# Performance work log

Measured on AMD Instinct MI355X. Metric: run time of the kernel, lower is better.

Reference implementation:

```python
import jax, jax.numpy as jnp
import numpy as np

HEADS = 16
HEAD_DIM = 64
HIDDEN = HEADS * HEAD_DIM  # 1024
COMPRESSION = 1.0  # concat([o, p], -1) forces compressed seq len == T, i.e. scale 1
LN_EPS = 1e-5


def _interp_linear_seq(x, scale):
    # F.interpolate(mode='linear', align_corners=False) along the sequence axis.
    # x: [B, T, C] -> [B, int(T*scale), C]
    T = x.shape[1]
    S = int(T * scale)
    src = (jnp.arange(S, dtype=jnp.float32) + 0.5) / scale - 0.5
    src = jnp.clip(src, 0.0, T - 1)
    lo = jnp.floor(src).astype(jnp.int32)
    hi = jnp.minimum(lo + 1, T - 1)
    w = (src - lo.astype(jnp.float32))[None, :, None]
    return x[:, lo] * (1.0 - w) + x[:, hi] * w


def _rotary(x):
    # rotate-half rotary embedding; x: [B, S, h, d]
    S, d = x.shape[1], x.shape[3]
    inv_freq = 1.0 / (10000.0 ** (jnp.arange(0, d, 2, dtype=jnp.float32) / d))
    ang = jnp.arange(S, dtype=jnp.float32)[:, None] * inv_freq  # [S, d/2]
    cos = jnp.cos(ang)[None, :, None, :]
    sin = jnp.sin(ang)[None, :, None, :]
    x1, x2 = jnp.split(x, 2, axis=-1)
    return jnp.concatenate([x1 * cos - x2 * sin, x1 * sin + x2 * cos], axis=-1)


def setup_inputs() -> dict:
    key = jax.random.key(0)
    ks = jax.random.split(key, 4)
    B, T = 4, 2048
    x = jax.random.normal(ks[0], (B, T, HIDDEN), dtype=jnp.float32)
    ln_gamma = jnp.ones((HIDDEN,), dtype=jnp.float32)
    ln_beta = jnp.zeros((HIDDEN,), dtype=jnp.float32)
    w_in = jax.random.normal(ks[1], (HIDDEN, 7 * HIDDEN), dtype=jnp.float32) * (HIDDEN ** -0.5)
    w_out = jax.random.normal(ks[2], (5 * HIDDEN, HIDDEN), dtype=jnp.float32) * ((5 * HIDDEN) ** -0.5)
    b_out = jnp.zeros((HIDDEN,), dtype=jnp.float32)
    return {"x": x, "ln_gamma": ln_gamma, "ln_beta": ln_beta,
            "w_in": w_in, "w_out": w_out, "b_out": b_out}


def reference(x, ln_gamma, ln_beta, w_in, w_out, b_out):
    B, T, _ = x.shape
    # LayerNorm
    mu = jnp.mean(x, axis=-1, keepdims=True)
    var = jnp.mean(jnp.square(x - mu), axis=-1, keepdims=True)
    xn = (x - mu) / jnp.sqrt(var + LN_EPS) * ln_gamma + ln_beta
    # fused QKVP projection (no bias)
    qkvp = xn @ w_in  # [B, T, 7*HIDDEN]
    q, k, v, p = jnp.split(qkvp, [HIDDEN, 2 * HIDDEN, 3 * HIDDEN], axis=-1)
    # linear-interpolation compression of k, v, p along the sequence axis
    k = _interp_linear_seq(k, COMPRESSION)
    v = _interp_linear_seq(v, COMPRESSION)
    p = _interp_linear_seq(p, COMPRESSION)
    S = k.shape[1]
    q = q.reshape(B, T, HEADS, HEAD_DIM)
    k = k.reshape(B, S, HEADS, HEAD_DIM)
    v = v.reshape(B, S, HEADS, HEAD_DIM)
    q = _rotary(q)
    k = _rotary(k)
    # manual softmax attention (no mask in the original)
    a = jnp.einsum('bihd,bjhd->bhij', q, k) * (HEAD_DIM ** -0.5)
    a = jax.nn.softmax(a, axis=-1)
    o = jnp.einsum('bhij,bjhd->bihd', a, v).reshape(B, T, HIDDEN)
    # GELU side branch (torch F.gelu default = exact erf gelu)
    p = jax.nn.gelu(p, approximate=False)
    return jnp.concatenate([o, p], axis=-1) @ w_out + b_out
```

## Files before the change

kernel.cpp:

```cpp
#include <hip/hip_runtime.h>
#include <hip/hip_bf16.h>
#include <math.h>

typedef short bf16x8 __attribute__((ext_vector_type(8)));
typedef float f32x4 __attribute__((ext_vector_type(4)));

#define HEADS 16
#define HDIM 64
#define HID 1024
#define B_ 4
#define T_ 2048
#define BT_ (B_*T_)
#define N1 (7*HID)
#define K2 (5*HID)

#define SM_SCALE_LOG2E 0.18033688011111793f

__device__ __forceinline__ float bf2f(unsigned short u) {
  union { unsigned int i; float f; } c; c.i = ((unsigned int)u) << 16; return c.f;
}
__device__ __forceinline__ unsigned short f2bf(float f) {
  __hip_bfloat16 h = __float2bfloat16(f);
  return __builtin_bit_cast(unsigned short, h);
}

typedef __attribute__((address_space(1))) const unsigned int gu32;
typedef __attribute__((address_space(3))) unsigned int lu32;
__device__ __forceinline__ void async16(const void* g, void* l) {
  __builtin_amdgcn_global_load_lds((gu32*)g, (lu32*)l, 16, 0, 0);
}

__global__ __launch_bounds__(256) void tcast_kernel(const float* __restrict__ in,
                                                    unsigned short* __restrict__ out,
                                                    int R, int C) {
  __shared__ float tile[64][65];
  int tx = threadIdx.x & 63;
  int ty = threadIdx.x >> 6;
  long r0 = (long)blockIdx.y * 64;
  long c0 = (long)blockIdx.x * 64;
#pragma unroll
  for (int i = 0; i < 16; i++) {
    int r = ty + i * 4;
    tile[r][tx] = in[(r0 + r) * C + c0 + tx];
  }
  __syncthreads();
#pragma unroll
  for (int i = 0; i < 16; i++) {
    int rr = ty + i * 4;
    out[(c0 + rr) * R + r0 + tx] = f2bf(tile[tx][rr]);
  }
}

__global__ __launch_bounds__(256) void ln_kernel(const float* __restrict__ x,
                                                 const float* __restrict__ g,
                                                 const float* __restrict__ b,
                                                 unsigned short* __restrict__ xn) {
  int row = blockIdx.x, tid = threadIdx.x;
  float4 v = reinterpret_cast<const float4*>(x + (long)row * HID)[tid];
  float s = v.x + v.y + v.z + v.w;
  float sq = v.x * v.x + v.y * v.y + v.z * v.z + v.w * v.w;
#pragma unroll
  for (int off = 32; off > 0; off >>= 1) { s += __shfl_down(s, off); sq += __shfl_down(sq, off); }
  __shared__ float red[8];
  int wid = tid >> 6, lane = tid & 63;
  if (lane == 0) { red[wid] = s; red[4 + wid] = sq; }
  __syncthreads();
  if (tid == 0) {
    red[0] = red[0] + red[1] + red[2] + red[3];
    red[4] = red[4] + red[5] + red[6] + red[7];
  }
  __syncthreads();
  float mean = red[0] * (1.f / HID);
  float var  = red[4] * (1.f / HID) - mean * mean;
  float rstd = rsqrtf(var + 1e-5f);
  float4 gv = reinterpret_cast<const float4*>(g)[tid];
  float4 bv = reinterpret_cast<const float4*>(b)[tid];
  ushort4 o;
  o.x = f2bf((v.x - mean) * rstd * gv.x + bv.x);
  o.y = f2bf((v.y - mean) * rstd * gv.y + bv.y);
  o.z = f2bf((v.z - mean) * rstd * gv.z + bv.z);
  o.w = f2bf((v.w - mean) * rstd * gv.w + bv.w);
  reinterpret_cast<ushort4*>(xn + (long)row * HID)[tid] = o;
}

__global__ __launch_bounds__(256) void gemm1_fused(const unsigned short* __restrict__ A,
                                                   const unsigned short* __restrict__ BT,
                                                   unsigned short* __restrict__ q_r,
                                                   unsigned short* __restrict__ k_r,
                                                   unsigned short* __restrict__ v_t,
                                                   unsigned short* __restrict__ C5) {
  __shared__ unsigned short As[128 * 32];
  __shared__ unsigned short Bs[128 * 32];
  __shared__ unsigned short Vt[4][64 * 72];
  int tid = threadIdx.x, lane = tid & 63, wid = tid >> 6;
  long row0 = (long)blockIdx.y * 128;
  long col0 = (long)blockIdx.x * 128;
  f32x4 acc[4][4] = {};
  int srow = lane >> 2;
  int scol = (lane & 3) * 8;
  for (int k0 = 0; k0 < HID; k0 += 32) {
#pragma unroll
    for (int i = 0; i < 2; i++) {
      int c = wid * 2 + i;
      async16(A  + (row0 + c * 16 + srow) * (long)HID + k0 + scol, &As[c * 512]);
      async16(BT + (col0 + c * 16 + srow) * (long)HID + k0 + scol, &Bs[c * 512]);
    }
    __syncthreads();
    int wm = (wid & 1) * 64, wn = (wid >> 1) * 64;
    bf16x8 af[4], bfv[4];
#pragma unroll
    for (int m = 0; m < 4; m++)
      af[m] = *reinterpret_cast<const bf16x8*>(&As[(wm + m * 16 + (lane & 15)) * 32 + (lane >> 4) * 8]);
#pragma unroll
    for (int n = 0; n < 4; n++)
      bfv[n] = *reinterpret_cast<const bf16x8*>(&Bs[(wn + n * 16 + (lane & 15)) * 32 + (lane >> 4) * 8]);
#pragma unroll
    for (int m = 0; m < 4; m++)
#pragma unroll
      for (int n = 0; n < 4; n++)
        acc[m][n] = __builtin_amdgcn_mfma_f32_16x16x32_bf16(af[m], bfv[n], acc[m][n], 0, 0, 0);
    __syncthreads();
  }
  int wm = (wid & 1) * 64, wn = (wid >> 1) * 64;
  long row_base = row0 + wm;
  int b = (int)(row_base >> 11);
  int t_base = (int)(row_base & 2047);
  int col_base = (int)col0 + wn;
  int region = col_base >> 10;
  int l15 = lane & 15, lq = lane >> 4;

  if (region <= 1) {
    unsigned short* dst = (region == 0) ? q_r : k_r;
    float osc = (region == 0) ? SM_SCALE_LOG2E : 1.0f;
    int head = (col_base & 1023) >> 6;
    long obase = (long)(b * 16 + head) * T_ * 64;
    float fr[2];
    fr[0] = __expf(-(float)l15 * 0.28782313662425572f);
    fr[1] = __expf(-(float)(16 + l15) * 0.28782313662425572f);
#pragma unroll
    for (int m = 0; m < 4; m++) {
#pragma unroll
      for (int j = 0; j < 4; j++) {
        int t = t_base + m * 16 + lq * 4 + j;
#pragma unroll
        for (int n = 0; n < 2; n++) {
          float sn, cs;
          sincosf((float)t * fr[n], &sn, &cs);
          float xl = acc[m][n][j], xh = acc[m][n + 2][j];
          int d = n * 16 + l15;
          dst[obase + (long)t * 64 + d]      = f2bf((xl * cs - xh * sn) * osc);
          dst[obase + (long)t * 64 + d + 32] = f2bf((xl * sn + xh * cs) * osc);
        }
      }
    }
  } else if (region == 2) {
    int head = (col_base & 1023) >> 6;
    unsigned short* vt = &Vt[wid][0];
#pragma unroll
    for (int m = 0; m < 4; m++)
#pragma unroll
      for (int n = 0; n < 4; n++)
#pragma unroll
        for (int j = 0; j < 4; j++)
          vt[(n * 16 + l15) * 72 + m * 16 + lq * 4 + j] = f2bf(acc[m][n][j]);
    long obase = (long)(b * 16 + head) * 64 * T_;
#pragma unroll
    for (int i = 0; i < 8; i++) {
      int d = i * 8 + (lane >> 3);
      int tl = (lane & 7) * 8;
      bf16x8 v = *reinterpret_cast<const bf16x8*>(&vt[d * 72 + tl]);
      *reinterpret_cast<bf16x8*>(v_t + obase + (long)d * T_ + t_base + tl) = v;
    }
  } else {
    int colp = col_base - 3 * HID;
#pragma unroll
    for (int m = 0; m < 4; m++) {
#pragma unroll
      for (int j = 0; j < 4; j++) {
        long row = row_base + m * 16 + lq * 4 + j;
#pragma unroll
        for (int n = 0; n < 4; n++) {
          float a = acc[m][n][j];
          float ga = 0.5f * a * (1.f + erff(a * 0.70710678118f));
          C5[row * K2 + HID + colp + n * 16 + l15] = f2bf(ga);
        }
      }
    }
  }
}

__global__ __launch_bounds__(256) void gemm_bt(const unsigned short* __restrict__ A,
                                               const unsigned short* __restrict__ BT,
                                               float* __restrict__ Cout,
                                               const float* __restrict__ bias,
                                               int K, int lda, int ldb, int ldc) {
  __shared__ unsigned short As[128 * 32];
  __shared__ unsigned short Bs[128 * 32];
  int tid = threadIdx.x, lane = tid & 63, wid = tid >> 6;
  long row0 = (long)blockIdx.y * 128;
  long col0 = (long)blockIdx.x * 128;
  f32x4 acc[4][4] = {};
  int srow = lane >> 2;
  int scol = (lane & 3) * 8;
  for (int k0 = 0; k0 < K; k0 += 32) {
#pragma unroll
    for (int i = 0; i < 2; i++) {
      int c = wid * 2 + i;
      async16(A  + (row0 + c * 16 + srow) * (long)lda + k0 + scol, &As[c * 512]);
      async16(BT + (col0 + c * 16 + srow) * (long)ldb + k0 + scol, &Bs[c * 512]);
    }
    __syncthreads();
    int wm = (wid & 1) * 64, wn = (wid >> 1) * 64;
    bf16x8 af[4], bfv[4];
#pragma unroll
    for (int m = 0; m < 4; m++)
      af[m] = *reinterpret_cast<const bf16x8*>(&As[(wm + m * 16 + (lane & 15)) * 32 + (lane >> 4) * 8]);
#pragma unroll
    for (int n = 0; n < 4; n++)
      bfv[n] = *reinterpret_cast<const bf16x8*>(&Bs[(wn + n * 16 + (lane & 15)) * 32 + (lane >> 4) * 8]);
#pragma unroll
    for (int m = 0; m < 4; m++)
#pragma unroll
      for (int n = 0; n < 4; n++)
        acc[m][n] = __builtin_amdgcn_mfma_f32_16x16x32_bf16(af[m], bfv[n], acc[m][n], 0, 0, 0);
    __syncthreads();
  }
  int wm = (wid & 1) * 64, wn = (wid >> 1) * 64;
#pragma unroll
  for (int m = 0; m < 4; m++) {
#pragma unroll
    for (int n = 0; n < 4; n++) {
      long r = row0 + wm + m * 16 + (lane >> 4) * 4;
      long c = col0 + wn + n * 16 + (lane & 15);
#pragma unroll
      for (int j = 0; j < 4; j++)
        Cout[(r + j) * (long)ldc + c] = acc[m][n][j] + bias[c];
    }
  }
}

__global__ __launch_bounds__(256) void attn_kernel(const unsigned short* __restrict__ q_r,
                                                   const unsigned short* __restrict__ k_r,
                                                   const unsigned short* __restrict__ v_t,
                                                   unsigned short* __restrict__ C5) {
  int qt = blockIdx.x;
  int bh = blockIdx.y;
  int b = bh >> 4, h = bh & 15;
  int tid = threadIdx.x, lane = tid & 63, wid = tid >> 6;
  int l15 = lane & 15, lq = lane >> 4;
  __shared__ unsigned short Ks[64 * 64];
  __shared__ unsigned short Vts[64 * 64];
  __shared__ unsigned short Ps[4][32 * 64];

  const unsigned short* qbase = q_r + ((long)bh * T_ + qt * 128 + wid * 32) * 64;
  bf16x8 aq[2][2];
#pragma unroll
  for (int m = 0; m < 2; m++)
#pragma unroll
    for (int kk = 0; kk < 2; kk++)
      aq[m][kk] = *reinterpret_cast<const bf16x8*>(
          qbase + (m * 16 + l15) * 64 + kk * 32 + lq * 8);

  f32x4 o_acc[2][4] = {};
  float l_run[2][4] = {};

  const unsigned short* kbase = k_r + (long)bh * T_ * 64;
  const unsigned short* vbase = v_t + (long)bh * 64 * T_;
  int srow = lane >> 3;
  int schnk = lane & 7;
  int slot = schnk ^ srow;
  unsigned short* Pw = &Ps[wid][0];

  bf16x8 kreg[2], vreg[2];
#pragma unroll
  for (int i = 0; i < 2; i++) {
    int c = wid * 2 + i;
    kreg[i] = *reinterpret_cast<const bf16x8*>(kbase + c * 512 + lane * 8);
    vreg[i] = *reinterpret_cast<const bf16x8*>(vbase + (long)(c * 8 + srow) * T_ + schnk * 8);
  }

  for (int kt = 0; kt < 32; kt++) {
#pragma unroll
    for (int i = 0; i < 2; i++) {
      int r = (wid * 2 + i) * 8 + srow;
      *reinterpret_cast<bf16x8*>(&Ks[r * 64 + slot * 8])  = kreg[i];
      *reinterpret_cast<bf16x8*>(&Vts[r * 64 + slot * 8]) = vreg[i];
    }
    if (kt < 31) {
#pragma unroll
      for (int i = 0; i < 2; i++) {
        int c = wid * 2 + i;
        kreg[i] = *reinterpret_cast<const bf16x8*>(kbase + (kt + 1) * 4096 + c * 512 + lane * 8);
        vreg[i] = *reinterpret_cast<const bf16x8*>(vbase + (long)(c * 8 + srow) * T_ + (kt + 1) * 64 + schnk * 8);
      }
    }
    __syncthreads();
    f32x4 s[2][4] = {};
#pragma unroll
    for (int n = 0; n < 4; n++) {
      int krow = n * 16 + l15;
      bf16x8 bk[2];
#pragma unroll
      for (int kk = 0; kk < 2; kk++)
        bk[kk] = *reinterpret_cast<const bf16x8*>(
            &Ks[krow * 64 + ((kk * 4 + lq) ^ (krow & 7)) * 8]);
#pragma unroll
      for (int m = 0; m < 2; m++)
#pragma unroll
        for (int kk = 0; kk < 2; kk++)
          s[m][n] = __builtin_amdgcn_mfma_f32_16x16x32_bf16(aq[m][kk], bk[kk], s[m][n], 0, 0, 0);
    }
#pragma unroll
    for (int m = 0; m < 2; m++)
#pragma unroll
      for (int n = 0; n < 4; n++)
#pragma unroll
        for (int j = 0; j < 4; j++) {
          float p = exp2f(s[m][n][j]);
          l_run[m][j] += p;
          int prow = m * 16 + lq * 4 + j;
          int pcol = n * 16 + l15;
          Pw[prow * 64 + (((pcol >> 3) ^ (prow & 7)) << 3) + (pcol & 7)] = f2bf(p);
        }
    bf16x8 ap[2][2];
#pragma unroll
    for (int m = 0; m < 2; m++)
#pragma unroll
      for (int kk = 0; kk < 2; kk++) {
        int prow = m * 16 + l15;
        ap[m][kk] = *reinterpret_cast<const bf16x8*>(
            &Pw[prow * 64 + (((kk * 4 + lq) ^ (prow & 7)) << 3)]);
      }
#pragma unroll
    for (int n = 0; n < 4; n++) {
      int vrow = n * 16 + l15;
      bf16x8 bv[2];
#pragma unroll
      for (int kk = 0; kk < 2; kk++)
        bv[kk] = *reinterpret_cast<const bf16x8*>(
            &Vts[vrow * 64 + ((kk * 4 + lq) ^ (vrow & 7)) * 8]);
#pragma unroll
      for (int m = 0; m < 2; m++)
#pragma unroll
        for (int kk = 0; kk < 2; kk++)
          o_acc[m][n] = __builtin_amdgcn_mfma_f32_16x16x32_bf16(ap[m][kk], bv[kk], o_acc[m][n], 0, 0, 0);
    }
    __syncthreads();
  }
#pragma unroll
  for (int m = 0; m < 2; m++)
#pragma unroll
    for (int j = 0; j < 4; j++) {
      float l = l_run[m][j];
      l += __shfl_xor(l, 1);
      l += __shfl_xor(l, 2);
      l += __shfl_xor(l, 4);
      l += __shfl_xor(l, 8);
      float inv = 1.0f / l;
      int tl = qt * 128 + wid * 32 + m * 16 + lq * 4 + j;
      long row = (long)b * T_ + tl;
#pragma unroll
      for (int n = 0; n < 4; n++) {
        int col = h * 64 + n * 16 + l15;
        C5[row * K2 + col] = f2bf(o_acc[m][n][j] * inv);
      }
    }
}

extern "C" void kernel_launch(void* const* d_in, const int* in_sizes, int n_in,
                              void* d_out, int out_size, void* d_ws, size_t ws_size,
                              hipStream_t stream) {
  const float* x     = (const float*)d_in[0];
  const float* g     = (const float*)d_in[1];
  const float* be    = (const float*)d_in[2];
  const float* w_in  = (const float*)d_in[3];
  const float* w_out = (const float*)d_in[4];
  const float* b_out = (const float*)d_in[5];
  float* out = (float*)d_out;

  char* ws = (char*)d_ws;
  size_t off = 0;
  auto alloc = [&](size_t bytes) {
    void* p = ws + off;
    off += (bytes + 255) & ~(size_t)255;
    return p;
  };
  unsigned short* xn     = (unsigned short*)alloc((size_t)BT_ * HID * 2);
  unsigned short* w_inT  = (unsigned short*)alloc((size_t)N1 * HID * 2);
  unsigned short* w_outT = (unsigned short*)alloc((size_t)HID * K2 * 2);
  unsigned short* q_rb   = (unsigned short*)alloc((size_t)BT_ * HID * 2);
  unsigned short* k_rb   = (unsigned short*)alloc((size_t)BT_ * HID * 2);
  unsigned short* v_tb   = (unsigned short*)alloc((size_t)BT_ * HID * 2);
  unsigned short* C5     = (unsigned short*)alloc((size_t)BT_ * K2 * 2);

  tcast_kernel<<<dim3(N1 / 64, HID / 64), 256, 0, stream>>>(w_in, w_inT, HID, N1);
  tcast_kernel<<<dim3(HID / 64, K2 / 64), 256, 0, stream>>>(w_out, w_outT, K2, HID);
  ln_kernel<<<BT_, 256, 0, stream>>>(x, g, be, xn);
  gemm1_fused<<<dim3(N1 / 128, BT_ / 128), 256, 0, stream>>>(xn, w_inT, q_rb, k_rb, v_tb, C5);
  attn_kernel<<<dim3(T_ / 128, 64), 256, 0, stream>>>(q_rb, k_rb, v_tb, C5);
  gemm_bt<<<dim3(HID / 128, BT_ / 128), 256, 0, stream>>>(C5, w_outT, out, b_out,
                                                          K2, K2, K2, HID);
}
```

Baseline: 476.9 us.

## Register-prefetch GEMM mainloop with swizzled LDS, fast sincos and tanh GELU

Replaces the direct global-to-LDS async loads in both GEMMs with a shared core that prefetches the next K-slice into registers while the current slice is consumed, and XOR-swizzles the LDS layout to cut bank conflicts on fragment reads. The rotary epilogue switches to the fast __sincosf intrinsic, and the exact erf GELU is replaced with a tanh-approximation GELU. The approximations add numerical error relative to the exact erf reference. The prefetch costs extra VGPRs, which may lower occupancy.

```diff
diff --git a/kernel.cpp b/kernel.cpp
--- a/kernel.cpp
+++ b/kernel.cpp
@@ -23,11 +23,11 @@
   __hip_bfloat16 h = __float2bfloat16(f);
   return __builtin_bit_cast(unsigned short, h);
 }
-
-typedef __attribute__((address_space(1))) const unsigned int gu32;
-typedef __attribute__((address_space(3))) unsigned int lu32;
-__device__ __forceinline__ void async16(const void* g, void* l) {
-  __builtin_amdgcn_global_load_lds((gu32*)g, (lu32*)l, 16, 0, 0);
+__device__ __forceinline__ float gelu_fast(float x) {
+  float y = 0.7978845608028654f * (x + 0.044715f * x * x * x);
+  float e = exp2f(y * 2.8853900817779268f);
+  float t = 1.f - 2.f / (e + 1.f);
+  return 0.5f * x * (1.f + t);
 }
 
 __global__ __launch_bounds__(256) void tcast_kernel(const float* __restrict__ in,
@@ -81,6 +81,60 @@
   o.z = f2bf((v.z - mean) * rstd * gv.z + bv.z);
   o.w = f2bf((v.w - mean) * rstd * gv.w + bv.w);
   reinterpret_cast<ushort4*>(xn + (long)row * HID)[tid] = o;
+}
+
+__device__ __forceinline__ void gemm_core32(const unsigned short* __restrict__ A,
+                                            const unsigned short* __restrict__ BT,
+                                            unsigned short* As, unsigned short* Bs,
+                                            int K, int lda, int ldb,
+                                            long row0, long col0,
+                                            int lane, int wid, f32x4 (&acc)[4][4]) {
+  int l15 = lane & 15, lq = lane >> 4;
+  int srow = lane >> 2;
+  int schnk = lane & 3;
+  int r0s = wid * 32 + srow;
+  int r1s = r0s + 16;
+  int slot0 = schnk ^ ((r0s >> 1) & 3);
+  int slot1 = schnk ^ ((r1s >> 1) & 3);
+  const unsigned short* a0 = A + (row0 + r0s) * (long)lda + schnk * 8;
+  const unsigned short* a1 = A + (row0 + r1s) * (long)lda + schnk * 8;
+  const unsigned short* b0 = BT + (col0 + r0s) * (long)ldb + schnk * 8;
+  const unsigned short* b1 = BT + (col0 + r1s) * (long)ldb + schnk * 8;
+  bf16x8 ar0 = *reinterpret_cast<const bf16x8*>(a0);
+  bf16x8 ar1 = *reinterpret_cast<const bf16x8*>(a1);
+  bf16x8 br0 = *reinterpret_cast<const bf16x8*>(b0);
+  bf16x8 br1 = *reinterpret_cast<const bf16x8*>(b1);
+  int wm = (wid & 1) * 64, wn = (wid >> 1) * 64;
+  for (int k0 = 0; k0 < K; k0 += 32) {
+    *reinterpret_cast<bf16x8*>(&As[r0s * 32 + slot0 * 8]) = ar0;
+    *reinterpret_cast<bf16x8*>(&As[r1s * 32 + slot1 * 8]) = ar1;
+    *reinterpret_cast<bf16x8*>(&Bs[r0s * 32 + slot0 * 8]) = br0;
+    *reinterpret_cast<bf16x8*>(&Bs[r1s * 32 + slot1 * 8]) = br1;
+    if (k0 + 32 < K) {
+      ar0 = *reinterpret_cast<const bf16x8*>(a0 + k0 + 32);
+      ar1 = *reinterpret_cast<const bf16x8*>(a1 + k0 + 32);
+      br0 = *reinterpret_cast<const bf16x8*>(b0 + k0 + 32);
+      br1 = *reinterpret_cast<const bf16x8*>(b1 + k0 + 32);
+    }
+    __syncthreads();
+    bf16x8 af[4], bfv[4];
+#pragma unroll
+    for (int m = 0; m < 4; m++) {
+      int r = wm + m * 16 + l15;
+      af[m] = *reinterpret_cast<const bf16x8*>(&As[r * 32 + (lq ^ ((r >> 1) & 3)) * 8]);
+    }
+#pragma unroll
+    for (int n = 0; n < 4; n++) {
+      int r = wn + n * 16 + l15;
+      bfv[n] = *reinterpret_cast<const bf16x8*>(&Bs[r * 32 + (lq ^ ((r >> 1) & 3)) * 8]);
+    }
+#pragma unroll
+    for (int m = 0; m < 4; m++)
+#pragma unroll
+      for (int n = 0; n < 4; n++)
+        acc[m][n] = __builtin_amdgcn_mfma_f32_16x16x32_bf16(af[m], bfv[n], acc[m][n], 0, 0, 0);
+    __syncthreads();
+  }
 }
 
 __global__ __launch_bounds__(256) void gemm1_fused(const unsigned short* __restrict__ A,
@@ -96,31 +150,8 @@
   long row0 = (long)blockIdx.y * 128;
   long col0 = (long)blockIdx.x * 128;
   f32x4 acc[4][4] = {};
-  int srow = lane >> 2;
-  int scol = (lane & 3) * 8;
-  for (int k0 = 0; k0 < HID; k0 += 32) {
-#pragma unroll
-    for (int i = 0; i < 2; i++) {
-      int c = wid * 2 + i;
-      async16(A  + (row0 + c * 16 + srow) * (long)HID + k0 + scol, &As[c * 512]);
-      async16(BT + (col0 + c * 16 + srow) * (long)HID + k0 + scol, &Bs[c * 512]);
-    }
-    __syncthreads();
-    int wm = (wid & 1) * 64, wn = (wid >> 1) * 64;
-    bf16x8 af[4], bfv[4];
-#pragma unroll
-    for (int m = 0; m < 4; m++)
-      af[m] = *reinterpret_cast<const bf16x8*>(&As[(wm + m * 16 + (lane & 15)) * 32 + (lane >> 4) * 8]);
-#pragma unroll
-    for (int n = 0; n < 4; n++)
-      bfv[n] = *reinterpret_cast<const bf16x8*>(&Bs[(wn + n * 16 + (lane & 15)) * 32 + (lane >> 4) * 8]);
-#pragma unroll
-    for (int m = 0; m < 4; m++)
-#pragma unroll
-      for (int n = 0; n < 4; n++)
-        acc[m][n] = __builtin_amdgcn_mfma_f32_16x16x32_bf16(af[m], bfv[n], acc[m][n], 0, 0, 0);
-    __syncthreads();
-  }
+  gemm_core32(A, BT, As, Bs, HID, HID, HID, row0, col0, lane, wid, acc);
+
   int wm = (wid & 1) * 64, wn = (wid >> 1) * 64;
   long row_base = row0 + wm;
   int b = (int)(row_base >> 11);
@@ -145,7 +176,7 @@
 #pragma unroll
         for (int n = 0; n < 2; n++) {
           float sn, cs;
-          sincosf((float)t * fr[n], &sn, &cs);
+          __sincosf((float)t * fr[n], &sn, &cs);
           float xl = acc[m][n][j], xh = acc[m][n + 2][j];
           int d = n * 16 + l15;
           dst[obase + (long)t * 64 + d]      = f2bf((xl * cs - xh * sn) * osc);
@@ -179,11 +210,8 @@
       for (int j = 0; j < 4; j++) {
         long row = row_base + m * 16 + lq * 4 + j;
 #pragma unroll
-        for (int n = 0; n < 4; n++) {
-          float a = acc[m][n][j];
-          float ga = 0.5f * a * (1.f + erff(a * 0.70710678118f));
-          C5[row * K2 + HID + colp + n * 16 + l15] = f2bf(ga);
-        }
+        for (int n = 0; n < 4; n++)
+          C5[row * K2 + HID + colp + n * 16 + l15] = f2bf(gelu_fast(acc[m][n][j]));
       }
     }
   }
@@ -200,31 +228,7 @@
   long row0 = (long)blockIdx.y * 128;
   long col0 = (long)blockIdx.x * 128;
   f32x4 acc[4][4] = {};
-  int srow = lane >> 2;
-  int scol = (lane & 3) * 8;
-  for (int k0 = 0; k0 < K; k0 += 32) {
-#pragma unroll
-    for (int i = 0; i < 2; i++) {
-      int c = wid * 2 + i;
-      async16(A  + (row0 + c * 16 + srow) * (long)lda + k0 + scol, &As[c * 512]);
-      async16(BT + (col0 + c * 16 + srow) * (long)ldb + k0 + scol, &Bs[c * 512]);
-    }
-    __syncthreads();
-    int wm = (wid & 1) * 64, wn = (wid >> 1) * 64;
-    bf16x8 af[4], bfv[4];
-#pragma unroll
-    for (int m = 0; m < 4; m++)
-      af[m] = *reinterpret_cast<const bf16x8*>(&As[(wm + m * 16 + (lane & 15)) * 32 + (lane >> 4) * 8]);
-#pragma unroll
-    for (int n = 0; n < 4; n++)
-      bfv[n] = *reinterpret_cast<const bf16x8*>(&Bs[(wn + n * 16 + (lane & 15)) * 32 + (lane >> 4) * 8]);
-#pragma unroll
-    for (int m = 0; m < 4; m++)
-#pragma unroll
-      for (int n = 0; n < 4; n++)
-        acc[m][n] = __builtin_amdgcn_mfma_f32_16x16x32_bf16(af[m], bfv[n], acc[m][n], 0, 0, 0);
-    __syncthreads();
-  }
+  gemm_core32(A, BT, As, Bs, K, lda, ldb, row0, col0, lane, wid, acc);
   int wm = (wid & 1) * 64, wn = (wid >> 1) * 64;
 #pragma unroll
   for (int m = 0; m < 4; m++) {
```

New measurement: 461.4 us. -3.2%, faster.
